# Optimization experiments

Measured on AMD Instinct MI355X. Metric: run time of the kernel, lower is better.

Reference implementation:

```python
import jax, jax.numpy as jnp
import numpy as np

IN_DIM, OUT_DIM = 64, 64
HIDDEN = [64, 64, 64]
D = IN_DIM * OUT_DIM  # number of independent per-edge small MLPs
B = 256


def setup_inputs() -> dict:
    key = jax.random.key(0)
    ks = jax.random.split(key, 10)

    def kaiming(k, shape, fan_in):
        # kaiming_uniform_ with a=0, nonlinearity='relu': bound = sqrt(6/fan_in)
        bound = np.sqrt(6.0 / fan_in)
        return jax.random.uniform(k, shape, jnp.float32, -bound, bound)

    def bias_init(k, shape, fan_in):
        bound = 1.0 / np.sqrt(fan_in)
        return jax.random.uniform(k, shape, jnp.float32, -bound, bound)

    h0, h1, h2 = HIDDEN
    inp = {
        "x": jax.random.normal(ks[0], (B, IN_DIM), jnp.float32),
        # Input_Linear: weight (out_dim, in_dim, h0); fan_in per torch kaiming on this tensor is in_dim*h0,
        # bias uses reset_parameters(1) -> fan_in=1
        "w0": kaiming(ks[1], (OUT_DIM, IN_DIM, h0), IN_DIM * h0),
        "b0": bias_init(ks[2], (D, h0), 1),
        # Linear(d, o=h1, i=h0): weight (d, h1, h0); kaiming fan_in = h0 (last dim), bias fan_in = i = h0
        "w1": kaiming(ks[3], (D, h1, h0), h0),
        "b1": bias_init(ks[4], (D, h1), h0),
        "w2": kaiming(ks[5], (D, h2, h1), h1),
        "b2": bias_init(ks[6], (D, h2), h1),
        # Output_Linear: weight (out_dim, in_dim*h2), fan_in = in_dim*h2
        "wout": kaiming(ks[7], (OUT_DIM, IN_DIM * h2), IN_DIM * h2),
        "bout": bias_init(ks[8], (OUT_DIM,), IN_DIM * h2),
    }
    return inp


def reference(x, w0, b0, w1, b1, w2, b2, wout, bout):
    Bsz = x.shape[0]
    # Input_Linear: broadcast outer product -> (B, out_dim, in_dim, h0) -> (B, d, h0)
    out = x[:, None, :, None] * w0[None, :, :, :]
    out = out.reshape(Bsz, D, HIDDEN[0]) + b0[None, :, :]
    out = jax.nn.relu(out)
    # Hidden per-edge Linear layers: 'doi,Bdi->Bdo'
    out = jnp.einsum('doi,bdi->bdo', w1, out) + b1[None, :, :]
    out = jax.nn.relu(out)
    out = jnp.einsum('doi,bdi->bdo', w2, out) + b2[None, :, :]
    out = jax.nn.relu(out)
    # Output_Linear: (B, d, h2) -> (B, out_dim, in_dim*h2); 'oi,boi->bo'
    xv = out.reshape(Bsz, OUT_DIM, IN_DIM * HIDDEN[-1])
    return jnp.einsum('oi,boi->bo', wout, xv) + bout[None, :]
```

## Files before the change

### kernel.cpp

```cpp
#include <hip/hip_runtime.h>
#include <hip/hip_bf16.h>


#define D_EDGES 4096

typedef __attribute__((ext_vector_type(4))) float f32x4;
typedef __attribute__((ext_vector_type(8))) short bf16x8;

__device__ __forceinline__ unsigned pk2(float a, float b) {
    __hip_bfloat162 h = __float22bfloat162_rn(float2{a, b});
    return *reinterpret_cast<unsigned*>(&h);
}

__global__ __launch_bounds__(256, 4) void kan_mfma(
    const float* __restrict__ x,
    const float* __restrict__ w0g,
    const float* __restrict__ b0g,
    const float* __restrict__ w1g,
    const float* __restrict__ b1g,
    const float* __restrict__ w2g,
    const float* __restrict__ b2g,
    const float* __restrict__ woutg,
    float* __restrict__ outbuf,
    int atomic_mode)
{
    const int d = blockIdx.x, o = d >> 6, ii = d & 63;
    const int t = threadIdx.x;
    const int lane = t & 63, wv = t >> 6;

    __shared__ __align__(16) unsigned char Hs[128 * 128];
    __shared__ __align__(16) unsigned char W1s[64 * 128];
    __shared__ __align__(16) unsigned char W2s[64 * 128];
    __shared__ __align__(16) float sx[256];
    __shared__ __align__(16) float sw0[64], sb0[64], sb1[64], sb2[64], swo[64];

    {
        const int orow = t >> 2, q = t & 3;
        const unsigned swz  = (unsigned)((orow & 7) << 4);
        const unsigned base = (unsigned)(orow * 128);
        const float* s1 = w1g + (size_t)d * 4096 + orow * 64 + q * 16;
        const float* s2 = w2g + (size_t)d * 4096 + orow * 64 + q * 16;

        float4 a0 = ((const float4*)s1)[0], a1 = ((const float4*)s1)[1];
        float4 a2 = ((const float4*)s1)[2], a3 = ((const float4*)s1)[3];
        uint4 u0 = { pk2(a0.x, a0.y), pk2(a0.z, a0.w), pk2(a1.x, a1.y), pk2(a1.z, a1.w) };
        uint4 u1 = { pk2(a2.x, a2.y), pk2(a2.z, a2.w), pk2(a3.x, a3.y), pk2(a3.z, a3.w) };
        *(uint4*)&W1s[base + ((unsigned)(q * 32)      ^ swz)] = u0;
        *(uint4*)&W1s[base + ((unsigned)(q * 32 + 16) ^ swz)] = u1;

        a0 = ((const float4*)s2)[0]; a1 = ((const float4*)s2)[1];
        a2 = ((const float4*)s2)[2]; a3 = ((const float4*)s2)[3];
        uint4 v0 = { pk2(a0.x, a0.y), pk2(a0.z, a0.w), pk2(a1.x, a1.y), pk2(a1.z, a1.w) };
        uint4 v1 = { pk2(a2.x, a2.y), pk2(a2.z, a2.w), pk2(a3.x, a3.y), pk2(a3.z, a3.w) };
        *(uint4*)&W2s[base + ((unsigned)(q * 32)      ^ swz)] = v0;
        *(uint4*)&W2s[base + ((unsigned)(q * 32 + 16) ^ swz)] = v1;
    }
    sx[t] = x[t * 64 + ii];
    if (t < 64) {
        sw0[t] = w0g[(size_t)d * 64 + t];
        sb0[t] = b0g[(size_t)d * 64 + t];
        sb1[t] = b1g[(size_t)d * 64 + t];
        sb2[t] = b2g[(size_t)d * 64 + t];
        swo[t] = woutg[(size_t)o * 4096 + ii * 64 + t];
    }
    __syncthreads();

    const f32x4 zero4 = { 0.f, 0.f, 0.f, 0.f };

    for (int hf = 0; hf < 2; ++hf) {
        {
            const int m  = t & 127;
            const int cb = (t >> 7) * 32;
            const float xb = sx[hf * 128 + m];
            const unsigned swz = (unsigned)((m & 7) << 4);
            const unsigned rb  = (unsigned)(m * 128);
#pragma unroll
            for (int c = 0; c < 4; ++c) {
                const int j = cb + c * 8;
                float4 wA = *(const float4*)&sw0[j];
                float4 wB = *(const float4*)&sw0[j + 4];
                float4 bA = *(const float4*)&sb0[j];
                float4 bB = *(const float4*)&sb0[j + 4];
                float v0 = fmaxf(fmaf(xb, wA.x, bA.x), 0.f);
                float v1 = fmaxf(fmaf(xb, wA.y, bA.y), 0.f);
                float v2 = fmaxf(fmaf(xb, wA.z, bA.z), 0.f);
                float v3 = fmaxf(fmaf(xb, wA.w, bA.w), 0.f);
                float v4 = fmaxf(fmaf(xb, wB.x, bB.x), 0.f);
                float v5 = fmaxf(fmaf(xb, wB.y, bB.y), 0.f);
                float v6 = fmaxf(fmaf(xb, wB.z, bB.z), 0.f);
                float v7 = fmaxf(fmaf(xb, wB.w, bB.w), 0.f);
                uint4 u = { pk2(v0, v1), pk2(v2, v3), pk2(v4, v5), pk2(v6, v7) };
                *(uint4*)&Hs[rb + ((unsigned)(2 * j) ^ swz)] = u;
            }
        }
        __syncthreads();

        const int arow = lane & 15;
        const int kb   = (lane >> 4) * 16;
        const unsigned lswz = (unsigned)((lane & 7) << 4);

        f32x4 acc[2][4];
#pragma unroll
        for (int i = 0; i < 2; ++i)
#pragma unroll
            for (int j = 0; j < 4; ++j) acc[i][j] = zero4;
        {
            bf16x8 wf[4][2];
#pragma unroll
            for (int nt = 0; nt < 4; ++nt)
#pragma unroll
                for (int ks = 0; ks < 2; ++ks)
                    wf[nt][ks] = *(const bf16x8*)&W1s[(nt * 16 + arow) * 128 +
                                    ((unsigned)(ks * 64 + kb) ^ lswz)];
#pragma unroll
            for (int mt2 = 0; mt2 < 2; ++mt2) {
                const unsigned rb = (unsigned)(((wv * 2 + mt2) * 16 + arow) * 128);
#pragma unroll
                for (int ks = 0; ks < 2; ++ks) {
                    bf16x8 bh = *(const bf16x8*)&Hs[rb + ((unsigned)(ks * 64 + kb) ^ lswz)];
#pragma unroll
                    for (int nt = 0; nt < 4; ++nt)
                        acc[mt2][nt] = __builtin_amdgcn_mfma_f32_16x16x32_bf16(
                            wf[nt][ks], bh, acc[mt2][nt], 0, 0, 0);
                }
            }
        }
        __syncthreads();

        {
            const int r0 = (lane >> 4) * 4;
#pragma unroll
            for (int mt2 = 0; mt2 < 2; ++mt2) {
                const int m = (wv * 2 + mt2) * 16 + arow;
                const unsigned rb  = (unsigned)(m * 128);
                const unsigned swz = (unsigned)((m & 7) << 4);
#pragma unroll
                for (int nt = 0; nt < 4; ++nt) {
                    float4 bv = *(const float4*)&sb1[nt * 16 + r0];
                    float v0 = fmaxf(acc[mt2][nt][0] + bv.x, 0.f);
                    float v1 = fmaxf(acc[mt2][nt][1] + bv.y, 0.f);
                    float v2 = fmaxf(acc[mt2][nt][2] + bv.z, 0.f);
                    float v3 = fmaxf(acc[mt2][nt][3] + bv.w, 0.f);
                    uint2 hp = { pk2(v0, v1), pk2(v2, v3) };
                    *(uint2*)&Hs[rb + ((unsigned)(2 * (nt * 16 + r0)) ^ swz)] = hp;
                }
            }
        }
        __syncthreads();

        f32x4 acc2[2][4];
#pragma unroll
        for (int i = 0; i < 2; ++i)
#pragma unroll
            for (int j = 0; j < 4; ++j) acc2[i][j] = zero4;
        {
            bf16x8 wf[4][2];
#pragma unroll
            for (int nt = 0; nt < 4; ++nt)
#pragma unroll
                for (int ks = 0; ks < 2; ++ks)
                    wf[nt][ks] = *(const bf16x8*)&W2s[(nt * 16 + arow) * 128 +
                                    ((unsigned)(ks * 64 + kb) ^ lswz)];
#pragma unroll
            for (int mt2 = 0; mt2 < 2; ++mt2) {
                const unsigned rb = (unsigned)(((wv * 2 + mt2) * 16 + arow) * 128);
#pragma unroll
                for (int ks = 0; ks < 2; ++ks) {
                    bf16x8 bh = *(const bf16x8*)&Hs[rb + ((unsigned)(ks * 64 + kb) ^ lswz)];
#pragma unroll
                    for (int nt = 0; nt < 4; ++nt)
                        acc2[mt2][nt] = __builtin_amdgcn_mfma_f32_16x16x32_bf16(
                            wf[nt][ks], bh, acc2[mt2][nt], 0, 0, 0);
                }
            }
        }

        {
            const int r0 = (lane >> 4) * 4;
#pragma unroll
            for (int mt2 = 0; mt2 < 2; ++mt2) {
                float p = 0.f;
#pragma unroll
                for (int nt = 0; nt < 4; ++nt) {
                    float4 bv = *(const float4*)&sb2[nt * 16 + r0];
                    float4 wo = *(const float4*)&swo[nt * 16 + r0];
                    p = fmaf(fmaxf(acc2[mt2][nt][0] + bv.x, 0.f), wo.x, p);
                    p = fmaf(fmaxf(acc2[mt2][nt][1] + bv.y, 0.f), wo.y, p);
                    p = fmaf(fmaxf(acc2[mt2][nt][2] + bv.z, 0.f), wo.z, p);
                    p = fmaf(fmaxf(acc2[mt2][nt][3] + bv.w, 0.f), wo.w, p);
                }
                p += __shfl_xor(p, 16);
                p += __shfl_xor(p, 32);
                const int b = hf * 128 + (wv * 2 + mt2) * 16 + arow;
                if (lane < 16) {
                    if (atomic_mode) atomicAdd(&outbuf[b * 64 + o], p);
                    else             outbuf[(size_t)d * 256 + b] = p;
                }
            }
        }
        __syncthreads();
    }
}

__global__ __launch_bounds__(256) void kan_reduce(
    const float* __restrict__ partial,
    const float* __restrict__ bout,
    float* __restrict__ y)
{
    const int o = blockIdx.x;
    const int b = threadIdx.x;
    float acc = bout[o];
    const float* p = partial + (size_t)o * (64 * 256) + b;
#pragma unroll
    for (int i = 0; i < 64; ++i)
        acc += p[i * 256];
    y[b * 64 + o] = acc;
}

__global__ __launch_bounds__(256) void kan_init_out(const float* __restrict__ bout,
                                                    float* __restrict__ y)
{
    const int idx = blockIdx.x * 256 + threadIdx.x;
    y[idx] = bout[idx & 63];
}

extern "C" void kernel_launch(void* const* d_in, const int* in_sizes, int n_in,
                              void* d_out, int out_size, void* d_ws, size_t ws_size,
                              hipStream_t stream) {
    const float* x    = (const float*)d_in[0];
    const float* w0   = (const float*)d_in[1];
    const float* b0   = (const float*)d_in[2];
    const float* w1   = (const float*)d_in[3];
    const float* b1   = (const float*)d_in[4];
    const float* w2   = (const float*)d_in[5];
    const float* b2   = (const float*)d_in[6];
    const float* wout = (const float*)d_in[7];
    const float* bout = (const float*)d_in[8];
    float* y = (float*)d_out;

    const size_t partial_bytes = (size_t)D_EDGES * 256 * sizeof(float);

    if (ws_size >= partial_bytes) {
        float* partial = (float*)d_ws;
        kan_mfma<<<D_EDGES, 256, 0, stream>>>(x, w0, b0, w1, b1, w2, b2, wout, partial, 0);
        kan_reduce<<<64, 256, 0, stream>>>(partial, bout, y);
    } else {
        kan_init_out<<<64, 256, 0, stream>>>(bout, y);
        kan_mfma<<<D_EDGES, 256, 0, stream>>>(x, w0, b0, w1, b1, w2, b2, wout, y, 1);
    }
}
```

Measured before the change: 45.59 us.

## Compute layer-0 activations in registers and give each wave private batch rows

Layer 0 (outer product plus bias and ReLU) is now computed directly in registers as the MFMA B operand instead of being staged through shared memory. The batch is no longer split into two halves: each wave owns 64 batch rows over the full 256-row batch, with a larger shared H buffer. Because each wave only reads back the H rows it wrote itself, the block-wide barriers in the main loop are replaced by a wave-local LDS wait. Accumulators double in size and shared memory grows, so launch bounds drop to 3 blocks per CU, which lowers occupancy in exchange for fewer barriers and less LDS traffic.

```diff
diff --git a/kernel.cpp b/kernel.cpp
--- a/kernel.cpp
+++ b/kernel.cpp
@@ -12,7 +12,9 @@
     return *reinterpret_cast<unsigned*>(&h);
 }
 
-__global__ __launch_bounds__(256, 4) void kan_mfma(
+union BFr { unsigned u[4]; bf16x8 v; };
+
+__global__ __launch_bounds__(256, 3) void kan_mfma(
     const float* __restrict__ x,
     const float* __restrict__ w0g,
     const float* __restrict__ b0g,
@@ -28,9 +30,9 @@
     const int t = threadIdx.x;
     const int lane = t & 63, wv = t >> 6;
 
-    __shared__ __align__(16) unsigned char Hs[128 * 128];
     __shared__ __align__(16) unsigned char W1s[64 * 128];
     __shared__ __align__(16) unsigned char W2s[64 * 128];
+    __shared__ __align__(16) unsigned char Hs[256 * 128];
     __shared__ __align__(16) float sx[256];
     __shared__ __align__(16) float sw0[64], sb0[64], sb1[64], sb2[64], swo[64];
 
@@ -65,140 +67,125 @@
     }
     __syncthreads();
 
+    const int arow = lane & 15;
+    const int kb   = (lane >> 4) * 16;
+    const int g8   = (lane >> 4) * 8;
+    const unsigned lswz = (unsigned)((lane & 7) << 4);
+    const int mbase = wv * 64;
+    const int r0 = (lane >> 4) * 4;
     const f32x4 zero4 = { 0.f, 0.f, 0.f, 0.f };
 
-    for (int hf = 0; hf < 2; ++hf) {
-        {
-            const int m  = t & 127;
-            const int cb = (t >> 7) * 32;
-            const float xb = sx[hf * 128 + m];
-            const unsigned swz = (unsigned)((m & 7) << 4);
-            const unsigned rb  = (unsigned)(m * 128);
-#pragma unroll
-            for (int c = 0; c < 4; ++c) {
-                const int j = cb + c * 8;
-                float4 wA = *(const float4*)&sw0[j];
-                float4 wB = *(const float4*)&sw0[j + 4];
-                float4 bA = *(const float4*)&sb0[j];
-                float4 bB = *(const float4*)&sb0[j + 4];
-                float v0 = fmaxf(fmaf(xb, wA.x, bA.x), 0.f);
-                float v1 = fmaxf(fmaf(xb, wA.y, bA.y), 0.f);
-                float v2 = fmaxf(fmaf(xb, wA.z, bA.z), 0.f);
-                float v3 = fmaxf(fmaf(xb, wA.w, bA.w), 0.f);
-                float v4 = fmaxf(fmaf(xb, wB.x, bB.x), 0.f);
-                float v5 = fmaxf(fmaf(xb, wB.y, bB.y), 0.f);
-                float v6 = fmaxf(fmaf(xb, wB.z, bB.z), 0.f);
-                float v7 = fmaxf(fmaf(xb, wB.w, bB.w), 0.f);
-                uint4 u = { pk2(v0, v1), pk2(v2, v3), pk2(v4, v5), pk2(v6, v7) };
-                *(uint4*)&Hs[rb + ((unsigned)(2 * j) ^ swz)] = u;
-            }
-        }
-        __syncthreads();
-
-        const int arow = lane & 15;
-        const int kb   = (lane >> 4) * 16;
-        const unsigned lswz = (unsigned)((lane & 7) << 4);
-
-        f32x4 acc[2][4];
-#pragma unroll
-        for (int i = 0; i < 2; ++i)
-#pragma unroll
-            for (int j = 0; j < 4; ++j) acc[i][j] = zero4;
-        {
-            bf16x8 wf[4][2];
+    bf16x8 wf1[4][2];
+#pragma unroll
+    for (int nt = 0; nt < 4; ++nt)
+#pragma unroll
+        for (int ks = 0; ks < 2; ++ks)
+            wf1[nt][ks] = *(const bf16x8*)&W1s[(nt * 16 + arow) * 128 +
+                            ((unsigned)(ks * 64 + kb) ^ lswz)];
+
+    float4 w0v[2][2], b0v[2][2];
+#pragma unroll
+    for (int ks = 0; ks < 2; ++ks) {
+        const int k0 = ks * 32 + g8;
+        w0v[ks][0] = *(const float4*)&sw0[k0];
+        w0v[ks][1] = *(const float4*)&sw0[k0 + 4];
+        b0v[ks][0] = *(const float4*)&sb0[k0];
+        b0v[ks][1] = *(const float4*)&sb0[k0 + 4];
+    }
+
+    f32x4 acc[4][4];
+#pragma unroll
+    for (int i = 0; i < 4; ++i)
+#pragma unroll
+        for (int j = 0; j < 4; ++j) acc[i][j] = zero4;
+
+#pragma unroll
+    for (int mti = 0; mti < 4; ++mti) {
+        const float xm = sx[mbase + mti * 16 + arow];
+#pragma unroll
+        for (int ks = 0; ks < 2; ++ks) {
+            float4 wa = w0v[ks][0], wb = w0v[ks][1];
+            float4 ba = b0v[ks][0], bb = b0v[ks][1];
+            float v0 = fmaxf(fmaf(xm, wa.x, ba.x), 0.f);
+            float v1 = fmaxf(fmaf(xm, wa.y, ba.y), 0.f);
+            float v2 = fmaxf(fmaf(xm, wa.z, ba.z), 0.f);
+            float v3 = fmaxf(fmaf(xm, wa.w, ba.w), 0.f);
+            float v4 = fmaxf(fmaf(xm, wb.x, bb.x), 0.f);
+            float v5 = fmaxf(fmaf(xm, wb.y, bb.y), 0.f);
+            float v6 = fmaxf(fmaf(xm, wb.z, bb.z), 0.f);
+            float v7 = fmaxf(fmaf(xm, wb.w, bb.w), 0.f);
+            BFr bh;
+            bh.u[0] = pk2(v0, v1); bh.u[1] = pk2(v2, v3);
+            bh.u[2] = pk2(v4, v5); bh.u[3] = pk2(v6, v7);
 #pragma unroll
             for (int nt = 0; nt < 4; ++nt)
-#pragma unroll
-                for (int ks = 0; ks < 2; ++ks)
-                    wf[nt][ks] = *(const bf16x8*)&W1s[(nt * 16 + arow) * 128 +
-                                    ((unsigned)(ks * 64 + kb) ^ lswz)];
-#pragma unroll
-            for (int mt2 = 0; mt2 < 2; ++mt2) {
-                const unsigned rb = (unsigned)(((wv * 2 + mt2) * 16 + arow) * 128);
-#pragma unroll
-                for (int ks = 0; ks < 2; ++ks) {
-                    bf16x8 bh = *(const bf16x8*)&Hs[rb + ((unsigned)(ks * 64 + kb) ^ lswz)];
-#pragma unroll
-                    for (int nt = 0; nt < 4; ++nt)
-                        acc[mt2][nt] = __builtin_amdgcn_mfma_f32_16x16x32_bf16(
-                            wf[nt][ks], bh, acc[mt2][nt], 0, 0, 0);
-                }
-            }
-        }
-        __syncthreads();
-
-        {
-            const int r0 = (lane >> 4) * 4;
-#pragma unroll
-            for (int mt2 = 0; mt2 < 2; ++mt2) {
-                const int m = (wv * 2 + mt2) * 16 + arow;
-                const unsigned rb  = (unsigned)(m * 128);
-                const unsigned swz = (unsigned)((m & 7) << 4);
-#pragma unroll
-                for (int nt = 0; nt < 4; ++nt) {
-                    float4 bv = *(const float4*)&sb1[nt * 16 + r0];
-                    float v0 = fmaxf(acc[mt2][nt][0] + bv.x, 0.f);
-                    float v1 = fmaxf(acc[mt2][nt][1] + bv.y, 0.f);
-                    float v2 = fmaxf(acc[mt2][nt][2] + bv.z, 0.f);
-                    float v3 = fmaxf(acc[mt2][nt][3] + bv.w, 0.f);
-                    uint2 hp = { pk2(v0, v1), pk2(v2, v3) };
-                    *(uint2*)&Hs[rb + ((unsigned)(2 * (nt * 16 + r0)) ^ swz)] = hp;
-                }
-            }
-        }
-        __syncthreads();
-
-        f32x4 acc2[2][4];
-#pragma unroll
-        for (int i = 0; i < 2; ++i)
-#pragma unroll
-            for (int j = 0; j < 4; ++j) acc2[i][j] = zero4;
-        {
-            bf16x8 wf[4][2];
+                acc[mti][nt] = __builtin_amdgcn_mfma_f32_16x16x32_bf16(
+                    wf1[nt][ks], bh.v, acc[mti][nt], 0, 0, 0);
+        }
+    }
+
+#pragma unroll
+    for (int mti = 0; mti < 4; ++mti) {
+        const unsigned rb = (unsigned)((mbase + mti * 16 + arow) * 128);
+#pragma unroll
+        for (int nt = 0; nt < 4; ++nt) {
+            float4 bv = *(const float4*)&sb1[nt * 16 + r0];
+            float v0 = fmaxf(acc[mti][nt][0] + bv.x, 0.f);
+            float v1 = fmaxf(acc[mti][nt][1] + bv.y, 0.f);
+            float v2 = fmaxf(acc[mti][nt][2] + bv.z, 0.f);
+            float v3 = fmaxf(acc[mti][nt][3] + bv.w, 0.f);
+            uint2 hp = { pk2(v0, v1), pk2(v2, v3) };
+            *(uint2*)&Hs[rb + ((unsigned)(2 * (nt * 16 + r0)) ^ lswz)] = hp;
+        }
+    }
+
+    asm volatile("s_waitcnt lgkmcnt(0)" ::: "memory");
+
+    bf16x8 wf2[4][2];
+#pragma unroll
+    for (int nt = 0; nt < 4; ++nt)
+#pragma unroll
+        for (int ks = 0; ks < 2; ++ks)
+            wf2[nt][ks] = *(const bf16x8*)&W2s[(nt * 16 + arow) * 128 +
+                            ((unsigned)(ks * 64 + kb) ^ lswz)];
+
+#pragma unroll
+    for (int i = 0; i < 4; ++i)
+#pragma unroll
+        for (int j = 0; j < 4; ++j) acc[i][j] = zero4;
+
+#pragma unroll
+    for (int mti = 0; mti < 4; ++mti) {
+        const unsigned rb = (unsigned)((mbase + mti * 16 + arow) * 128);
+#pragma unroll
+        for (int ks = 0; ks < 2; ++ks) {
+            bf16x8 bh = *(const bf16x8*)&Hs[rb + ((unsigned)(ks * 64 + kb) ^ lswz)];
 #pragma unroll
             for (int nt = 0; nt < 4; ++nt)
-#pragma unroll
-                for (int ks = 0; ks < 2; ++ks)
-                    wf[nt][ks] = *(const bf16x8*)&W2s[(nt * 16 + arow) * 128 +
-                                    ((unsigned)(ks * 64 + kb) ^ lswz)];
-#pragma unroll
-            for (int mt2 = 0; mt2 < 2; ++mt2) {
-                const unsigned rb = (unsigned)(((wv * 2 + mt2) * 16 + arow) * 128);
-#pragma unroll
-                for (int ks = 0; ks < 2; ++ks) {
-                    bf16x8 bh = *(const bf16x8*)&Hs[rb + ((unsigned)(ks * 64 + kb) ^ lswz)];
-#pragma unroll
-                    for (int nt = 0; nt < 4; ++nt)
-                        acc2[mt2][nt] = __builtin_amdgcn_mfma_f32_16x16x32_bf16(
-                            wf[nt][ks], bh, acc2[mt2][nt], 0, 0, 0);
-                }
-            }
-        }
-
-        {
-            const int r0 = (lane >> 4) * 4;
-#pragma unroll
-            for (int mt2 = 0; mt2 < 2; ++mt2) {
-                float p = 0.f;
-#pragma unroll
-                for (int nt = 0; nt < 4; ++nt) {
-                    float4 bv = *(const float4*)&sb2[nt * 16 + r0];
-                    float4 wo = *(const float4*)&swo[nt * 16 + r0];
-                    p = fmaf(fmaxf(acc2[mt2][nt][0] + bv.x, 0.f), wo.x, p);
-                    p = fmaf(fmaxf(acc2[mt2][nt][1] + bv.y, 0.f), wo.y, p);
-                    p = fmaf(fmaxf(acc2[mt2][nt][2] + bv.z, 0.f), wo.z, p);
-                    p = fmaf(fmaxf(acc2[mt2][nt][3] + bv.w, 0.f), wo.w, p);
-                }
-                p += __shfl_xor(p, 16);
-                p += __shfl_xor(p, 32);
-                const int b = hf * 128 + (wv * 2 + mt2) * 16 + arow;
-                if (lane < 16) {
-                    if (atomic_mode) atomicAdd(&outbuf[b * 64 + o], p);
-                    else             outbuf[(size_t)d * 256 + b] = p;
-                }
-            }
-        }
-        __syncthreads();
+                acc[mti][nt] = __builtin_amdgcn_mfma_f32_16x16x32_bf16(
+                    wf2[nt][ks], bh, acc[mti][nt], 0, 0, 0);
+        }
+    }
+
+#pragma unroll
+    for (int mti = 0; mti < 4; ++mti) {
+        float p = 0.f;
+#pragma unroll
+        for (int nt = 0; nt < 4; ++nt) {
+            float4 bv = *(const float4*)&sb2[nt * 16 + r0];
+            float4 wo = *(const float4*)&swo[nt * 16 + r0];
+            p = fmaf(fmaxf(acc[mti][nt][0] + bv.x, 0.f), wo.x, p);
+            p = fmaf(fmaxf(acc[mti][nt][1] + bv.y, 0.f), wo.y, p);
+            p = fmaf(fmaxf(acc[mti][nt][2] + bv.z, 0.f), wo.z, p);
+            p = fmaf(fmaxf(acc[mti][nt][3] + bv.w, 0.f), wo.w, p);
+        }
+        p += __shfl_xor(p, 16);
+        p += __shfl_xor(p, 32);
+        const int b = mbase + mti * 16 + arow;
+        if (lane < 16) {
+            if (atomic_mode) atomicAdd(&outbuf[b * 64 + o], p);
+            else             outbuf[(size_t)d * 256 + b] = p;
+        }
     }
 }
 
```

Result: faster. 43.25 us (-5.1%).
